# Optimization experiments

Hardware: AMD Instinct MI355X
Metric: run time of the kernel (lower is better)

## Reference

```python
import jax, jax.numpy as jnp
import numpy as np

B, L = 256, 100
N100, N10_100, N0_10 = 40000, 80000, 120000
D100, D10_100, D0_10 = 500, 250, 250  # layers[0]/2, layers[0]/4, remainder
H1, H2 = 200, 1000                    # layers = [1000, 200, 1000]
NUM_PIX = N100 + N10_100 + N0_10


def setup_inputs() -> dict:
    key = jax.random.key(0)
    ks = jax.random.split(key, 11)
    rn = lambda k, shape, scale: jax.random.normal(k, shape, jnp.float32) * scale
    return {
        'songs_bucket': jax.random.randint(ks[0], (B, L), 0, 3, jnp.int32),
        'songs_id': jax.random.randint(ks[1], (B, L), 0, N100, jnp.int32),
        'W100': rn(ks[2], (N100, D100), 0.02),
        'W10_100': rn(ks[3], (N10_100, D10_100), 0.02),
        'W0_10': rn(ks[4], (N0_10, D0_10), 0.02),
        'fc1_w': rn(ks[5], (H1, 1000), 0.03),
        'fc1_b': jnp.zeros((H1,), jnp.float32),
        'fc2_w': rn(ks[6], (H2, H1), 0.07),
        'fc2_b': jnp.zeros((H2,), jnp.float32),
        'out_w': rn(ks[7], (NUM_PIX, H2), 0.03),
        'out_b': jnp.zeros((NUM_PIX,), jnp.float32),
    }


def _masked_mean(table, ids, mask):
    # table: [V, D], ids: [B, L], mask: [B, L] bool -> [B, D]
    emb = table[ids]                                   # gather [B, L, D]
    m = mask.astype(emb.dtype)
    ssum = jnp.einsum('bl,bld->bd', m, emb)            # masked segment-sum
    cnt = m.sum(axis=1)                                # [B]
    mean = ssum / jnp.maximum(cnt, 1.0)[:, None]
    return jnp.where(cnt[:, None] > 0, mean, 0.0)     # empty bucket -> zeros


def reference(songs_bucket, songs_id, W100, W10_100, W0_10,
              fc1_w, fc1_b, fc2_w, fc2_b, out_w, out_b):
    # per-bucket masked embedding mean (vectorized embedding-bag)
    e0 = _masked_mean(W100, songs_id, songs_bucket == 0)       # [B, 500]
    e1 = _masked_mean(W10_100, songs_id, songs_bucket == 1)    # [B, 250]
    e2 = _masked_mean(W0_10, songs_id, songs_bucket == 2)      # [B, 250]
    x = jnp.concatenate([e0, e1, e2], axis=-1)                 # [B, 1000]
    # tiny MLP (dropout p=False -> p=0, a no-op)
    h = jax.nn.relu(x @ fc1_w.T + fc1_b)                       # [B, 200]
    h = jax.nn.relu(h @ fc2_w.T + fc2_b)                       # [B, 1000]
    ratings = h @ out_w.T + out_b                              # [B, NUM_PIX]
    return ratings
```

## Files before the change

kernel.cpp:

```cpp
#include <hip/hip_runtime.h>

#define NUM_B 256
#define SEQ_L 100
#define NPIX  240000
#define KPAD  1024
#define BN    64
#define BK    128
#define NWG   3750

typedef __attribute__((ext_vector_type(8))) short short8;
typedef __attribute__((ext_vector_type(4))) float f32x4;

static __device__ __forceinline__ unsigned short f2bf(float f) {
  unsigned int u = __builtin_bit_cast(unsigned int, f);
  u += 0x7fffu + ((u >> 16) & 1u);
  return (unsigned short)(u >> 16);
}

__global__ __launch_bounds__(1024) void embed_mlp_kernel(
    const int* __restrict__ bucket, const int* __restrict__ ids,
    const float* __restrict__ W100, const float* __restrict__ W10,
    const float* __restrict__ W0,
    const float* __restrict__ fc1_w, const float* __restrict__ fc1_b,
    const float* __restrict__ fc2_w, const float* __restrict__ fc2_b,
    unsigned short* __restrict__ h2out)
{
  __shared__ __align__(16) float xw[16][1000];
  __shared__ __align__(16) float xs[1000];
  __shared__ __align__(16) float h1s[200];
  __shared__ int sb[SEQ_L], sid[SEQ_L];
  __shared__ int cnt[16][3];
  __shared__ int cntT[3];

  const int row = blockIdx.x, tid = threadIdx.x;
  const int wid = tid >> 6, lane = tid & 63;

  if (tid < SEQ_L) {
    sb[tid]  = bucket[row * SEQ_L + tid];
    sid[tid] = ids[row * SEQ_L + tid];
  }
  __syncthreads();

  float acc0[8] = {0,0,0,0,0,0,0,0};
  float acc1[4] = {0,0,0,0};
  float acc2[4] = {0,0,0,0};
  int c0 = 0, c1 = 0, c2 = 0;

  for (int l = wid; l < SEQ_L; l += 16) {
    const int b = sb[l];
    const long id = sid[l];
    if (b == 0) {
      ++c0; const float* r = W100 + id * 500;
      #pragma unroll
      for (int j = 0; j < 7; ++j) acc0[j] += r[lane + 64 * j];
      if (lane < 52) acc0[7] += r[lane + 448];
    } else if (b == 1) {
      ++c1; const float* r = W10 + id * 250;
      #pragma unroll
      for (int j = 0; j < 3; ++j) acc1[j] += r[lane + 64 * j];
      if (lane < 58) acc1[3] += r[lane + 192];
    } else {
      ++c2; const float* r = W0 + id * 250;
      #pragma unroll
      for (int j = 0; j < 3; ++j) acc2[j] += r[lane + 64 * j];
      if (lane < 58) acc2[3] += r[lane + 192];
    }
  }
  {
    float* xp = xw[wid];
    #pragma unroll
    for (int j = 0; j < 8; ++j) { int d = lane + 64 * j; if (d < 500) xp[d] = acc0[j]; }
    #pragma unroll
    for (int j = 0; j < 4; ++j) { int d = lane + 64 * j; if (d < 250) xp[500 + d] = acc1[j]; }
    #pragma unroll
    for (int j = 0; j < 4; ++j) { int d = lane + 64 * j; if (d < 250) xp[750 + d] = acc2[j]; }
    if (lane == 0) { cnt[wid][0] = c0; cnt[wid][1] = c1; cnt[wid][2] = c2; }
  }
  __syncthreads();
  if (tid < 3) { int s = 0; for (int w = 0; w < 16; ++w) s += cnt[w][tid]; cntT[tid] = s; }
  __syncthreads();
  if (tid < 1000) {
    float s = 0.f;
    #pragma unroll
    for (int w = 0; w < 16; ++w) s += xw[w][tid];
    const int bkt = tid < 500 ? 0 : (tid < 750 ? 1 : 2);
    const int c = cntT[bkt];
    xs[tid] = c ? s / (float)c : 0.f;
  }
  __syncthreads();

  const int g = tid >> 4, sl = tid & 15;

  for (int o = g; o < 200; o += 64) {
    const f32x4* wr = (const f32x4*)(fc1_w + o * 1000);
    const f32x4* xv = (const f32x4*)xs;
    float p = 0.f;
    for (int j = sl; j < 250; j += 16) {
      f32x4 a = xv[j], b = wr[j];
      p += a.x * b.x + a.y * b.y + a.z * b.z + a.w * b.w;
    }
    #pragma unroll
    for (int off = 8; off; off >>= 1) p += __shfl_down(p, off, 16);
    if (sl == 0) h1s[o] = fmaxf(p + fc1_b[o], 0.f);
  }
  __syncthreads();

  unsigned short* hrow = h2out + (long)row * KPAD;
  for (int o = g; o < 1000; o += 64) {
    const f32x4* wr = (const f32x4*)(fc2_w + o * 200);
    const f32x4* hv = (const f32x4*)h1s;
    float p = 0.f;
    #pragma unroll
    for (int j = sl; j < 50; j += 16) {
      f32x4 a = hv[j], b = wr[j];
      p += a.x * b.x + a.y * b.y + a.z * b.z + a.w * b.w;
    }
    #pragma unroll
    for (int off = 8; off; off >>= 1) p += __shfl_down(p, off, 16);
    if (sl == 0) hrow[o] = f2bf(fmaxf(p + fc2_b[o], 0.f));
  }
  if (tid < KPAD - 1000) hrow[1000 + tid] = 0;
}

__global__ __launch_bounds__(512, 4) void out_gemm_kernel(
    const unsigned short* __restrict__ h2,
    const float* __restrict__ out_w,
    const float* __restrict__ out_b,
    float* __restrict__ out)
{
  __shared__ __align__(16) unsigned char lds[81920];
  unsigned char* As = lds;
  unsigned char* Bs = lds + 65536;

  const int tid = threadIdx.x;

  const int q = NWG / 8, r = NWG % 8;
  const int xcd = blockIdx.x & 7, bidx = blockIdx.x >> 3;
  const int wg = (xcd < r ? xcd * (q + 1) : r * (q + 1) + (xcd - r) * q) + bidx;
  const long n0 = (long)wg * BN;

  const f32x4 fz = {0.f, 0.f, 0.f, 0.f};

  f32x4 bReg[4];

  auto dmaA = [&](int kt) {
    #pragma unroll
    for (int i = 0; i < 8; ++i) {
      const int c = tid + 512 * i;
      const int rw = c >> 4;
      const int k16s = (c & 15) ^ (rw & 7);
      const unsigned short* src = h2 + rw * KPAD + kt * BK + k16s * 8;
      __builtin_amdgcn_global_load_lds(
          (const __attribute__((address_space(1))) void*)src,
          (__attribute__((address_space(3))) void*)(As + c * 16),
          16, 0, 0);
    }
  };
  auto loadB = [&](int k0) {
    #pragma unroll
    for (int i = 0; i < 4; ++i) {
      int c = tid + 512 * i;
      int n = c >> 5, qq = c & 31;
      int k = k0 + qq * 4;
      bReg[i] = (k < 1000)
        ? __builtin_nontemporal_load((const f32x4*)(out_w + (long)(n0 + n) * 1000 + k))
        : fz;
    }
  };
  auto storeB = [&]() {
    #pragma unroll
    for (int i = 0; i < 4; ++i) {
      int c = tid + 512 * i;
      int n = c >> 5, qq = c & 31;
      ushort4 h;
      h.x = f2bf(bReg[i].x); h.y = f2bf(bReg[i].y);
      h.z = f2bf(bReg[i].z); h.w = f2bf(bReg[i].w);
      *(ushort4*)(Bs + n * 256 + ((qq * 8) ^ ((n & 7) << 4))) = h;
    }
  };

  const int wid = tid >> 6, lane = tid & 63;
  const int wm = wid >> 1, wn = wid & 1;
  const int lrow = lane & 15, lkg = lane >> 4;

  f32x4 acc[4][2];
  #pragma unroll
  for (int m = 0; m < 4; ++m) { acc[m][0] = fz; acc[m][1] = fz; }

  dmaA(0); loadB(0);
  #pragma unroll 1
  for (int kt = 0; kt < 8; ++kt) {
    storeB();
    __syncthreads();
    if (kt < 7) loadB((kt + 1) * BK);
    #pragma unroll
    for (int kk = 0; kk < 4; ++kk) {
      short8 bf[2];
      #pragma unroll
      for (int n = 0; n < 2; ++n) {
        int nr = wn * 32 + n * 16 + lrow;
        bf[n] = *(const short8*)(Bs + nr * 256 + (((kk * 64) + lkg * 16) ^ ((nr & 7) << 4)));
      }
      #pragma unroll
      for (int m = 0; m < 4; ++m) {
        int rr = wm * 64 + m * 16 + lrow;
        short8 af = *(const short8*)(As + rr * 256 + (((kk * 64) + lkg * 16) ^ ((rr & 7) << 4)));
        acc[m][0] = __builtin_amdgcn_mfma_f32_16x16x32_bf16(af, bf[0], acc[m][0], 0, 0, 0);
        acc[m][1] = __builtin_amdgcn_mfma_f32_16x16x32_bf16(af, bf[1], acc[m][1], 0, 0, 0);
      }
    }
    __syncthreads();
    if (kt < 7) dmaA(kt + 1);
  }

  const float b0 = out_b[n0 + wn * 32 + lrow];
  const float b1 = out_b[n0 + wn * 32 + 16 + lrow];
  float* E = (float*)lds;
  #pragma unroll
  for (int half = 0; half < 2; ++half) {
    __syncthreads();
    if ((wm >> 1) == half) {
      #pragma unroll
      for (int m = 0; m < 4; ++m) {
        #pragma unroll
        for (int n = 0; n < 2; ++n) {
          const int col = wn * 32 + n * 16 + lrow;
          const float bias = n ? b1 : b0;
          #pragma unroll
          for (int rr = 0; rr < 4; ++rr) {
            const int rowl = (wm & 1) * 64 + m * 16 + lkg * 4 + rr;
            E[rowl * 68 + col] = acc[m][n][rr] + bias;
          }
        }
      }
    }
    __syncthreads();
    const int rbase = half * 128;
    #pragma unroll
    for (int s = 0; s < 4; ++s) {
      const int idx = tid + 512 * s;
      const int rowl = idx >> 4;
      const int c = (idx & 15) * 4;
      f32x4 v = *(const f32x4*)(E + rowl * 68 + c);
      *(f32x4*)(out + (long)(rbase + rowl) * NPIX + n0 + c) = v;
    }
  }
}

extern "C" void kernel_launch(void* const* d_in, const int* in_sizes, int n_in,
                              void* d_out, int out_size, void* d_ws, size_t ws_size,
                              hipStream_t stream) {
  const int*   bucket = (const int*)d_in[0];
  const int*   ids    = (const int*)d_in[1];
  const float* W100   = (const float*)d_in[2];
  const float* W10    = (const float*)d_in[3];
  const float* W0     = (const float*)d_in[4];
  const float* fc1w   = (const float*)d_in[5];
  const float* fc1b   = (const float*)d_in[6];
  const float* fc2w   = (const float*)d_in[7];
  const float* fc2b   = (const float*)d_in[8];
  const float* outw   = (const float*)d_in[9];
  const float* outb   = (const float*)d_in[10];
  float* out = (float*)d_out;
  unsigned short* h2w = (unsigned short*)d_ws;

  embed_mlp_kernel<<<NUM_B, 1024, 0, stream>>>(bucket, ids, W100, W10, W0,
                                               fc1w, fc1b, fc2w, fc2b, h2w);
  out_gemm_kernel<<<NWG, 512, 0, stream>>>(h2w, outw, outb, out);
}
```

Before: 333.7 us.

## Stream fp32 out_w tiles into double-buffered LDS via direct global-to-LDS DMA

The B operand (out_w) is now copied straight from global memory into LDS as fp32 with global_load_lds, instead of being staged through registers and converted to bf16 before the LDS store. The B tile is double-buffered, so the next tile's load overlaps the current tile's MFMA work, and the bf16 conversion moves to the point where fragments are read. Out-of-range k reads are clamped rather than zeroed, relying on the zero-padded A columns. In exchange, LDS per workgroup grows from 80KB to 128KB, which lowers occupancy, and each wave row group repeats the fp32-to-bf16 conversion on the same B data.

```diff
diff --git a/kernel.cpp b/kernel.cpp
--- a/kernel.cpp
+++ b/kernel.cpp
@@ -122,15 +122,13 @@
   if (tid < KPAD - 1000) hrow[1000 + tid] = 0;
 }
 
-__global__ __launch_bounds__(512, 4) void out_gemm_kernel(
+__global__ __launch_bounds__(512) void out_gemm_kernel(
     const unsigned short* __restrict__ h2,
     const float* __restrict__ out_w,
     const float* __restrict__ out_b,
     float* __restrict__ out)
 {
-  __shared__ __align__(16) unsigned char lds[81920];
-  unsigned char* As = lds;
-  unsigned char* Bs = lds + 65536;
+  __shared__ __align__(16) unsigned char lds[131072];
 
   const int tid = threadIdx.x;
 
@@ -138,10 +136,6 @@
   const int xcd = blockIdx.x & 7, bidx = blockIdx.x >> 3;
   const int wg = (xcd < r ? xcd * (q + 1) : r * (q + 1) + (xcd - r) * q) + bidx;
   const long n0 = (long)wg * BN;
-
-  const f32x4 fz = {0.f, 0.f, 0.f, 0.f};
-
-  f32x4 bReg[4];
 
   auto dmaA = [&](int kt) {
     #pragma unroll
@@ -152,30 +146,24 @@
       const unsigned short* src = h2 + rw * KPAD + kt * BK + k16s * 8;
       __builtin_amdgcn_global_load_lds(
           (const __attribute__((address_space(1))) void*)src,
-          (__attribute__((address_space(3))) void*)(As + c * 16),
+          (__attribute__((address_space(3))) void*)(lds + c * 16),
           16, 0, 0);
     }
   };
-  auto loadB = [&](int k0) {
+  auto dmaB = [&](int kt, int buf) {
+    unsigned char* dst = lds + 65536 + buf * 32768;
     #pragma unroll
     for (int i = 0; i < 4; ++i) {
-      int c = tid + 512 * i;
-      int n = c >> 5, qq = c & 31;
-      int k = k0 + qq * 4;
-      bReg[i] = (k < 1000)
-        ? __builtin_nontemporal_load((const f32x4*)(out_w + (long)(n0 + n) * 1000 + k))
-        : fz;
-    }
-  };
-  auto storeB = [&]() {
-    #pragma unroll
-    for (int i = 0; i < 4; ++i) {
-      int c = tid + 512 * i;
-      int n = c >> 5, qq = c & 31;
-      ushort4 h;
-      h.x = f2bf(bReg[i].x); h.y = f2bf(bReg[i].y);
-      h.z = f2bf(bReg[i].z); h.w = f2bf(bReg[i].w);
-      *(ushort4*)(Bs + n * 256 + ((qq * 8) ^ ((n & 7) << 4))) = h;
+      const int c = tid + 512 * i;
+      const int rw = c >> 5;
+      const int g  = (c & 31) ^ (rw & 7);
+      int k = kt * BK + g * 4;
+      if (k > 996) k = 996;
+      const float* src = out_w + (n0 + rw) * 1000 + k;
+      __builtin_amdgcn_global_load_lds(
+          (const __attribute__((address_space(1))) void*)src,
+          (__attribute__((address_space(3))) void*)(dst + c * 16),
+          16, 0, 0);
     }
   };
 
@@ -183,33 +171,47 @@
   const int wm = wid >> 1, wn = wid & 1;
   const int lrow = lane & 15, lkg = lane >> 4;
 
+  const f32x4 fz = {0.f, 0.f, 0.f, 0.f};
   f32x4 acc[4][2];
   #pragma unroll
   for (int m = 0; m < 4; ++m) { acc[m][0] = fz; acc[m][1] = fz; }
 
-  dmaA(0); loadB(0);
-  #pragma unroll 1
-  for (int kt = 0; kt < 8; ++kt) {
-    storeB();
-    __syncthreads();
-    if (kt < 7) loadB((kt + 1) * BK);
+  auto compute = [&](int buf) {
+    const unsigned char* Bb = lds + 65536 + buf * 32768;
     #pragma unroll
     for (int kk = 0; kk < 4; ++kk) {
       short8 bf[2];
       #pragma unroll
       for (int n = 0; n < 2; ++n) {
-        int nr = wn * 32 + n * 16 + lrow;
-        bf[n] = *(const short8*)(Bs + nr * 256 + (((kk * 64) + lkg * 16) ^ ((nr & 7) << 4)));
+        const int nr = wn * 32 + n * 16 + lrow;
+        const int x = kk * 128 + lkg * 32;
+        const int sw = (nr & 7) << 4;
+        f32x4 lo = *(const f32x4*)(Bb + nr * 512 + (x ^ sw));
+        f32x4 hi = *(const f32x4*)(Bb + nr * 512 + ((x + 16) ^ sw));
+        bf[n][0] = (short)f2bf(lo.x); bf[n][1] = (short)f2bf(lo.y);
+        bf[n][2] = (short)f2bf(lo.z); bf[n][3] = (short)f2bf(lo.w);
+        bf[n][4] = (short)f2bf(hi.x); bf[n][5] = (short)f2bf(hi.y);
+        bf[n][6] = (short)f2bf(hi.z); bf[n][7] = (short)f2bf(hi.w);
       }
       #pragma unroll
       for (int m = 0; m < 4; ++m) {
-        int rr = wm * 64 + m * 16 + lrow;
-        short8 af = *(const short8*)(As + rr * 256 + (((kk * 64) + lkg * 16) ^ ((rr & 7) << 4)));
+        const int rr = wm * 64 + m * 16 + lrow;
+        short8 af = *(const short8*)(lds + rr * 256 + (((kk * 64) + lkg * 16) ^ ((rr & 7) << 4)));
         acc[m][0] = __builtin_amdgcn_mfma_f32_16x16x32_bf16(af, bf[0], acc[m][0], 0, 0, 0);
         acc[m][1] = __builtin_amdgcn_mfma_f32_16x16x32_bf16(af, bf[1], acc[m][1], 0, 0, 0);
       }
     }
+  };
+
+  dmaA(0); dmaB(0, 0);
+  #pragma unroll 1
+  for (int kt = 0; kt < 8; ++kt) {
     __syncthreads();
+    if (kt < 7) dmaB(kt + 1, (kt + 1) & 1);
+    compute(kt & 1);
+    asm volatile("s_waitcnt lgkmcnt(0)" ::: "memory");
+    __builtin_amdgcn_s_barrier();
+    __builtin_amdgcn_sched_barrier(0);
     if (kt < 7) dmaA(kt + 1);
   }
 
```

After: 428.2 us. +28.3%, slower.

## Double the B k-tile to 256 and decouple A/B staging in out GEMM

Applied to the files above, without the earlier changes.

The output GEMM now stages B (out_w converted to bf16) in 256-wide k tiles, so each thread holds eight register vectors and B is stored to LDS only every other 128-wide sub-step, while A keeps its 128-wide DMA per sub-step. This halves the number of B store-and-sync rounds and makes each global load larger, aiming to hide memory latency better. The loop end uses a manual lgkmcnt wait plus a raw barrier instead of __syncthreads. LDS grows to 96KB and the occupancy hint in launch_bounds is dropped, which may cut concurrent workgroups per CU and increases register pressure.

```diff
diff --git a/kernel.cpp b/kernel.cpp
--- a/kernel.cpp
+++ b/kernel.cpp
@@ -5,7 +5,7 @@
 #define NPIX  240000
 #define KPAD  1024
 #define BN    64
-#define BK    128
+#define BK    256
 #define NWG   3750
 
 typedef __attribute__((ext_vector_type(8))) short short8;
@@ -122,13 +122,13 @@
   if (tid < KPAD - 1000) hrow[1000 + tid] = 0;
 }
 
-__global__ __launch_bounds__(512, 4) void out_gemm_kernel(
+__global__ __launch_bounds__(512) void out_gemm_kernel(
     const unsigned short* __restrict__ h2,
     const float* __restrict__ out_w,
     const float* __restrict__ out_b,
     float* __restrict__ out)
 {
-  __shared__ __align__(16) unsigned char lds[81920];
+  __shared__ __align__(16) unsigned char lds[98304];
   unsigned char* As = lds;
   unsigned char* Bs = lds + 65536;
 
@@ -141,41 +141,41 @@
 
   const f32x4 fz = {0.f, 0.f, 0.f, 0.f};
 
-  f32x4 bReg[4];
-
-  auto dmaA = [&](int kt) {
+  f32x4 bReg[8];
+
+  auto dmaA = [&](int sp) {
     #pragma unroll
     for (int i = 0; i < 8; ++i) {
       const int c = tid + 512 * i;
       const int rw = c >> 4;
       const int k16s = (c & 15) ^ (rw & 7);
-      const unsigned short* src = h2 + rw * KPAD + kt * BK + k16s * 8;
+      const unsigned short* src = h2 + rw * KPAD + sp * 128 + k16s * 8;
       __builtin_amdgcn_global_load_lds(
           (const __attribute__((address_space(1))) void*)src,
           (__attribute__((address_space(3))) void*)(As + c * 16),
           16, 0, 0);
     }
   };
-  auto loadB = [&](int k0) {
-    #pragma unroll
-    for (int i = 0; i < 4; ++i) {
+  auto loadB = [&](int bt) {
+    #pragma unroll
+    for (int i = 0; i < 8; ++i) {
       int c = tid + 512 * i;
-      int n = c >> 5, qq = c & 31;
-      int k = k0 + qq * 4;
+      int rw = c >> 6, g4 = c & 63;
+      int k = bt * BK + g4 * 4;
       bReg[i] = (k < 1000)
-        ? __builtin_nontemporal_load((const f32x4*)(out_w + (long)(n0 + n) * 1000 + k))
+        ? __builtin_nontemporal_load((const f32x4*)(out_w + (n0 + rw) * 1000 + k))
         : fz;
     }
   };
   auto storeB = [&]() {
     #pragma unroll
-    for (int i = 0; i < 4; ++i) {
+    for (int i = 0; i < 8; ++i) {
       int c = tid + 512 * i;
-      int n = c >> 5, qq = c & 31;
+      int rw = c >> 6, g4 = c & 63;
       ushort4 h;
       h.x = f2bf(bReg[i].x); h.y = f2bf(bReg[i].y);
       h.z = f2bf(bReg[i].z); h.w = f2bf(bReg[i].w);
-      *(ushort4*)(Bs + n * 256 + ((qq * 8) ^ ((n & 7) << 4))) = h;
+      *(ushort4*)(Bs + rw * 512 + ((g4 * 8) ^ ((rw & 7) << 4))) = h;
     }
   };
 
@@ -187,19 +187,15 @@
   #pragma unroll
   for (int m = 0; m < 4; ++m) { acc[m][0] = fz; acc[m][1] = fz; }
 
-  dmaA(0); loadB(0);
-  #pragma unroll 1
-  for (int kt = 0; kt < 8; ++kt) {
-    storeB();
-    __syncthreads();
-    if (kt < 7) loadB((kt + 1) * BK);
+  auto compute = [&](int sp) {
+    const int kh = (sp & 1) * 256;
     #pragma unroll
     for (int kk = 0; kk < 4; ++kk) {
       short8 bf[2];
       #pragma unroll
       for (int n = 0; n < 2; ++n) {
         int nr = wn * 32 + n * 16 + lrow;
-        bf[n] = *(const short8*)(Bs + nr * 256 + (((kk * 64) + lkg * 16) ^ ((nr & 7) << 4)));
+        bf[n] = *(const short8*)(Bs + nr * 512 + ((kh + kk * 64 + lkg * 16) ^ ((nr & 7) << 4)));
       }
       #pragma unroll
       for (int m = 0; m < 4; ++m) {
@@ -209,8 +205,19 @@
         acc[m][1] = __builtin_amdgcn_mfma_f32_16x16x32_bf16(af, bf[1], acc[m][1], 0, 0, 0);
       }
     }
+  };
+
+  dmaA(0); loadB(0);
+  #pragma unroll 1
+  for (int sp = 0; sp < 8; ++sp) {
+    if (!(sp & 1)) storeB();
     __syncthreads();
-    if (kt < 7) dmaA(kt + 1);
+    if (!(sp & 1) && sp < 6) loadB((sp >> 1) + 1);
+    compute(sp);
+    asm volatile("s_waitcnt lgkmcnt(0)" ::: "memory");
+    __builtin_amdgcn_s_barrier();
+    __builtin_amdgcn_sched_barrier(0);
+    if (sp < 7) dmaA(sp + 1);
   }
 
   const float b0 = out_b[n0 + wn * 32 + lrow];
```

New measurement: 392.5 us. +17.6%, slower.
